# Kernel tuning notes

Hardware: AMD Instinct MI355X
Metric: run time of the kernel (lower is better)

Reference implementation:

```python
import jax, jax.numpy as jnp
import numpy as np

EPS = 1e-6  # torch.nn.CosineSimilarity eps


def _emb_sum(table, ids):
    # ids: (N, L) int -> (N, D): gather rows then sum over tokens (EmbeddingBag-sum)
    return table[ids].sum(axis=1)


def _cos_rows(q, M):
    # cosine similarity of vector q (D,) against each row of M (N, D), torch eps semantics:
    # dot / max(||a||*||b||, eps)
    num = M @ q
    den = jnp.maximum(jnp.linalg.norm(M, axis=1) * jnp.linalg.norm(q), EPS)
    return num / den


def setup_inputs() -> dict:
    key = jax.random.key(0)
    ks = jax.random.split(key, 10)
    V, D = 50000, 128
    N_MEM, N_CAND, N_PERS, L, LQ = 65536, 10000, 20, 20, 32
    return {
        "xs": jax.random.randint(ks[0], (1, LQ), 0, V, dtype=jnp.int32),
        "candidates": jax.random.randint(ks[1], (N_CAND, L), 0, V, dtype=jnp.int32),
        "persona": jax.random.randint(ks[2], (N_PERS, L), 0, V, dtype=jnp.int32),
        "keys": jax.random.randint(ks[3], (N_MEM, L), 0, V, dtype=jnp.int32),
        "values": jax.random.randint(ks[4], (N_MEM, L), 0, V, dtype=jnp.int32),
        "label": jax.random.randint(ks[5], (1, LQ), 0, V, dtype=jnp.int32),
        "shared_emb": jax.random.normal(ks[6], (V, D), dtype=jnp.float32),
        "cand_emb": jax.random.normal(ks[7], (V, D), dtype=jnp.float32),
        "R_W": jax.random.normal(ks[8], (D, D), dtype=jnp.float32) * (1.0 / np.sqrt(D)),
        "R2_W": jax.random.normal(ks[9], (D, D), dtype=jnp.float32) * (1.0 / np.sqrt(D)),
    }


def reference(xs, candidates, persona, keys, values, label, shared_emb, cand_emb, R_W, R2_W):
    enc_keys = _emb_sum(shared_emb, keys)        # (N_mem, D)
    enc_values = _emb_sum(shared_emb, values)    # (N_mem, D)
    enc_cands = _emb_sum(cand_emb, candidates)   # (N_cand, D)
    enc_pers = _emb_sum(shared_emb, persona)     # (N_pers, D)

    q = shared_emb[xs].sum(axis=1).reshape(-1)   # (D,)

    for W in (R_W, R2_W):  # loop is hardcoded to 2 hops in the source
        att = jax.nn.softmax(_cos_rows(q, enc_pers))          # (N_pers,)
        hop = (att[:, None] * enc_pers).sum(axis=0)           # (D,)
        q_plus = (q + hop) @ W.T                               # Linear no bias
        att = jax.nn.softmax(_cos_rows(q_plus, enc_keys))     # (N_mem,)
        hop = (att[:, None] * enc_values).sum(axis=0)         # (D,)
        q = (q_plus + hop) @ W.T

    preds = _cos_rows(q, enc_cands)  # (N_cand,)
    return preds
```

## Files before the change

kernel.cpp:

```cpp
#include <hip/hip_runtime.h>
#include <math.h>
#include <stdint.h>

#define D 128
#define EPS 1e-6f
typedef unsigned short u16;

#define NBK 16
#define BSTR 132
#define H1OFF 512
#define H2OFF (512 + NBK * BSTR)


__device__ __forceinline__ float wave_sum(float v) {
#pragma unroll
    for (int off = 32; off > 0; off >>= 1) v += __shfl_xor(v, off, 64);
    return v;
}
__device__ __forceinline__ float halfwave_sum(float v) {
#pragma unroll
    for (int off = 16; off > 0; off >>= 1) v += __shfl_xor(v, off, 32);
    return v;
}

__device__ __forceinline__ float bf2f(u16 h) {
    union { unsigned u; float f; } x;
    x.u = ((unsigned)h) << 16;
    return x.f;
}
__device__ __forceinline__ float bflo(unsigned u) { return bf2f((u16)(u & 0xffff)); }
__device__ __forceinline__ float bfhi(unsigned u) { return bf2f((u16)(u >> 16)); }
__device__ __forceinline__ u16 f2bf(float f) {
    union { float f; unsigned u; } x;
    x.f = f;
    unsigned u = x.u;
    return (u16)((u + 0x7fff + ((u >> 16) & 1)) >> 16);
}
__device__ __forceinline__ unsigned pack2(float a, float b) {
    return (unsigned)f2bf(a) | ((unsigned)f2bf(b) << 16);
}

__global__ void prep_k(const float* __restrict__ semb, u16* __restrict__ tbl,
                       int V, const int* __restrict__ pers, int NP,
                       const int* __restrict__ xs, int LQ,
                       float* __restrict__ enc_pers, float* __restrict__ pnorms,
                       float* __restrict__ st, int nbA) {
    const int tid = threadIdx.x;
    const int bid = blockIdx.x;
    if (bid < nbA) {
        const int n = V * 64;
        const int stride = nbA * 256;
        for (int i = bid * 256 + tid; i < n; i += stride) {
            const int v = i >> 6;
            const int c2 = i & 63;
            const float2 ab = *(const float2*)(semb + (long)v * D + 2 * c2);
            *(unsigned*)(tbl + (long)v * D + 2 * c2) = pack2(ab.x, ab.y);
        }
    } else {
        const int lane = tid & 63;
        const int half = lane >> 5;
        const int hl = lane & 31;
        const int w0 = (bid - nbA) * 4 + (tid >> 6);
        const int npr = NP + 1;
        const int npairs = (npr + 1) >> 1;
        for (int w = w0; w < npairs; w += 12) {
            const int row = 2 * w + half;
            const bool valid = row < npr;
            const int rowc = valid ? row : NP;
            const bool isq = (rowc == NP);
            const int* ids = isq ? xs : (pers + (long)rowc * 20);
            const int L = isq ? LQ : 20;
            int myid = 0;
            if (hl < L) myid = ids[hl];
            float4 acc = {0.f, 0.f, 0.f, 0.f};
            for (int t = 0; t < L; ++t) {
                const int idx = __shfl(myid, (half << 5) + t, 64);
                const float4 e = *(const float4*)(semb + (long)idx * D + 4 * hl);
                acc.x += e.x; acc.y += e.y; acc.z += e.z; acc.w += e.w;
            }
            if (valid) {
                float* outp = isq ? st : (enc_pers + (long)rowc * D);
                *(float4*)(outp + 4 * hl) = acc;
                float sq = acc.x * acc.x + acc.y * acc.y + acc.z * acc.z + acc.w * acc.w;
                sq = halfwave_sum(sq);
                if (hl == 0) {
                    if (isq) st[384] = sqrtf(sq);
                    else pnorms[rowc] = sqrtf(sq);
                }
            }
        }
    }
}

__device__ void persona_dev(const float* __restrict__ pers_rows,
                            const float* __restrict__ pnorms,
                            const float* __restrict__ W, float* __restrict__ st,
                            int NP, float* smem, int tid, int zb) {
    float* qsh = smem;
    float* qh = smem + 128;
    float* att = smem + 256;
    float* red = smem + 320;
    if (tid < D) qsh[tid] = st[tid];
    __syncthreads();
    if (tid < NP) {
        float dot = 0.f;
        const float* pr = pers_rows + (long)tid * D;
        for (int d2 = 0; d2 < D; ++d2) dot += pr[d2] * qsh[d2];
        att[tid] = dot / fmaxf(pnorms[tid] * st[384], EPS);
    }
    __syncthreads();
    if (tid == 0) {
        float m = -1e30f;
        for (int p = 0; p < NP; ++p) m = fmaxf(m, att[p]);
        float s = 0.f;
        for (int p = 0; p < NP; ++p) { att[p] = __expf(att[p] - m); s += att[p]; }
        float inv = 1.f / s;
        for (int p = 0; p < NP; ++p) att[p] *= inv;
    }
    __syncthreads();
    if (tid < D) {
        float h = 0.f;
        for (int p = 0; p < NP; ++p) h += att[p] * pers_rows[(long)p * D + tid];
        qh[tid] = qsh[tid] + h;
    }
    __syncthreads();
    float qp = 0.f;
    if (tid < D) {
        for (int d2 = 0; d2 < D; ++d2) qp += W[(long)tid * D + d2] * qh[d2];
        st[128 + tid] = qp;
    }
    float sq = wave_sum(qp * qp);
    if ((tid & 63) == 0 && tid < 128) red[tid >> 6] = sq;
    __syncthreads();
    if (tid == 0) st[385] = sqrtf(red[0] + red[1]);
    if (zb) {
        for (int i = tid; i < 2 * NBK * BSTR; i += (int)blockDim.x)
            st[H1OFF + i] = 0.f;
    } else {
        if (tid < D) st[256 + tid] = 0.f;
        if (tid == 0) st[386] = 0.f;
    }
}

__device__ void mid_dev_s(const float* __restrict__ W1, const float* __restrict__ W2,
                          const float* __restrict__ pers_rows,
                          const float* __restrict__ pnorms,
                          const float* __restrict__ st,
                          float* __restrict__ qp_out, float* __restrict__ qpn_out,
                          float* smem, int tid, int NP) {
    float* qh = smem;
    float* qsh = smem + 128;
    float* att = smem + 256;
    float* red = smem + 320;
    float esum = 0.f;
#pragma unroll
    for (int b = 0; b < NBK; ++b) esum += st[H1OFF + b * BSTR + 128];
    const float inv = 1.f / esum;
    if (tid < D) {
        float a = 0.f;
#pragma unroll
        for (int b = 0; b < NBK; ++b) a += st[H1OFF + b * BSTR + tid];
        qh[tid] = st[128 + tid] + a * inv;
    }
    __syncthreads();
    float qn = 0.f;
    if (tid < D) {
        for (int d2 = 0; d2 < D; ++d2) qn += W1[(long)tid * D + d2] * qh[d2];
        qsh[tid] = qn;
    }
    float sq = wave_sum(qn * qn);
    if ((tid & 63) == 0 && tid < 128) red[tid >> 6] = sq;
    __syncthreads();
    const float qnorm = sqrtf(red[0] + red[1]);
    if (tid < NP) {
        float dot = 0.f;
        for (int d2 = 0; d2 < D; ++d2) dot += pers_rows[(long)tid * D + d2] * qsh[d2];
        att[tid] = dot / fmaxf(pnorms[tid] * qnorm, EPS);
    }
    __syncthreads();
    if (tid == 0) {
        float m = -1e30f;
        for (int p = 0; p < NP; ++p) m = fmaxf(m, att[p]);
        float s = 0.f;
        for (int p = 0; p < NP; ++p) { att[p] = __expf(att[p] - m); s += att[p]; }
        float is = 1.f / s;
        for (int p = 0; p < NP; ++p) att[p] *= is;
    }
    __syncthreads();
    if (tid < D) {
        float h = 0.f;
        for (int p = 0; p < NP; ++p) h += att[p] * pers_rows[(long)p * D + tid];
        qh[tid] = qsh[tid] + h;
    }
    __syncthreads();
    float qp = 0.f;
    if (tid < D) {
        for (int d2 = 0; d2 < D; ++d2) qp += W2[(long)tid * D + d2] * qh[d2];
        qp_out[tid] = qp;
    }
    float sq2 = wave_sum(qp * qp);
    if ((tid & 63) == 0 && tid < 128) red[tid >> 6] = sq2;
    __syncthreads();
    if (tid == 0) *qpn_out = sqrtf(red[0] + red[1]);
    __syncthreads();
}

__global__ void kv_k(const u16* __restrict__ tbl, const int* __restrict__ kids,
                     int N, float* __restrict__ kb, float* __restrict__ knorms,
                     const float* __restrict__ enc_pers,
                     const float* __restrict__ pnorms,
                     const float* __restrict__ RW, float* __restrict__ st,
                     int NP) {
    __shared__ float smem[336];
    const int tid = threadIdx.x;
    const int bid = blockIdx.x;
    if (bid == 0) {
        persona_dev(enc_pers, pnorms, RW, st, NP, smem, tid, 1);
        return;
    }
    const int lane = tid & 63;
    const int half = lane >> 5;
    const int hl = lane & 31;
    const int ghw = ((bid - 1) * 256 + tid) >> 5;
    const int nhw = ((gridDim.x - 1) * 256) >> 5;
    for (int i = ghw; i < N; i += nhw) {
        int kid = 0;
        if (hl < 20) kid = kids[(long)i * 20 + hl];
        float k0 = 0.f, k1 = 0.f, k2 = 0.f, k3 = 0.f;
#pragma unroll
        for (int t = 0; t < 20; ++t) {
            const int kj = __shfl(kid, (half << 5) + t, 64);
            const ushort4 ke = *(const ushort4*)(tbl + (long)kj * D + 4 * hl);
            k0 += bf2f(ke.x); k1 += bf2f(ke.y); k2 += bf2f(ke.z); k3 += bf2f(ke.w);
        }
        float4 kr;
        kr.x = k0; kr.y = k1; kr.z = k2; kr.w = k3;
        *(float4*)(kb + (long)i * D + 4 * hl) = kr;
        float sq = halfwave_sum(k0 * k0 + k1 * k1 + k2 * k2 + k3 * k3);
        if (hl == 0) knorms[i] = sqrtf(sq);
    }
}

__global__ void kv_v(const u16* __restrict__ tbl, const int* __restrict__ vids,
                     int N, u16* __restrict__ vb) {
    const int tid = threadIdx.x;
    const int bid = blockIdx.x;
    const int lane = tid & 63;
    const int half = lane >> 5;
    const int hl = lane & 31;
    const int ghw = (bid * 256 + tid) >> 5;
    const int nhw = (gridDim.x * 256) >> 5;
    for (int i = ghw; i < N; i += nhw) {
        int vid = 0;
        if (hl < 20) vid = vids[(long)i * 20 + hl];
        float v0 = 0.f, v1 = 0.f, v2 = 0.f, v3 = 0.f;
#pragma unroll
        for (int t = 0; t < 20; ++t) {
            const int vj = __shfl(vid, (half << 5) + t, 64);
            const ushort4 ve = *(const ushort4*)(tbl + (long)vj * D + 4 * hl);
            v0 += bf2f(ve.x); v1 += bf2f(ve.y); v2 += bf2f(ve.z); v3 += bf2f(ve.w);
        }
        uint2 pv;
        pv.x = pack2(v0, v1);
        pv.y = pack2(v2, v3);
        *(uint2*)(vb + (long)i * D + 4 * hl) = pv;
    }
}

__global__ void attcv2_k(const float* __restrict__ kb, const u16* __restrict__ vb,
                         const float* __restrict__ knorms,
                         const float* __restrict__ W1, const float* __restrict__ W2,
                         const float* __restrict__ enc_pers,
                         const float* __restrict__ pnorms,
                         float* __restrict__ st, int N, int NP, int hop) {
    __shared__ float msm[324];
    __shared__ float qp_s[128];
    __shared__ float qpn_s;
    __shared__ float rsm[129];
    const int tid = threadIdx.x;
    if (hop == 0) {
        if (tid < 128) qp_s[tid] = st[128 + tid];
        if (tid == 0) qpn_s = st[385];
    } else {
        mid_dev_s(W1, W2, enc_pers, pnorms, st, qp_s, &qpn_s, msm, tid, NP);
    }
    __syncthreads();
    const int lane = tid & 63;
    const int half = lane >> 5;
    const int hl = lane & 31;
    const float4 qp4 = *(const float4*)(qp_s + 4 * hl);
    const float qpn = qpn_s;
    const int aoff = (hop ? H2OFF : H1OFF) + (int)(blockIdx.x & (NBK - 1)) * BSTR;
    const int ghw = (int)((blockIdx.x * blockDim.x + tid) >> 5);
    const int nhw = (int)((gridDim.x * blockDim.x) >> 5);
    float a0 = 0.f, a1 = 0.f, a2 = 0.f, a3 = 0.f;
    float esum = 0.f;
    for (int i = ghw; i < N; i += nhw) {
        const float4 kr = *(const float4*)(kb + (long)i * D + 4 * hl);
        const float part = kr.x * qp4.x + kr.y * qp4.y + kr.z * qp4.z + kr.w * qp4.w;
        const float dot = halfwave_sum(part);
        const float c = dot / fmaxf(knorms[i] * qpn, EPS);
        const float e = __expf(c);
        const uint2 vh = *(const uint2*)(vb + (long)i * D + 4 * hl);
        a0 += e * bflo(vh.x);
        a1 += e * bfhi(vh.x);
        a2 += e * bflo(vh.y);
        a3 += e * bfhi(vh.y);
        if (hl == 0) esum += e;
    }
    a0 += __shfl_xor(a0, 32, 64);
    a1 += __shfl_xor(a1, 32, 64);
    a2 += __shfl_xor(a2, 32, 64);
    a3 += __shfl_xor(a3, 32, 64);
    esum += __shfl_xor(esum, 32, 64);
    if (tid < 129) rsm[tid] = 0.f;
    __syncthreads();
    if (half == 0) {
        atomicAdd(&rsm[4 * hl + 0], a0);
        atomicAdd(&rsm[4 * hl + 1], a1);
        atomicAdd(&rsm[4 * hl + 2], a2);
        atomicAdd(&rsm[4 * hl + 3], a3);
        if (hl == 0) atomicAdd(&rsm[128], esum);
    }
    __syncthreads();
    if (tid < 128) atomicAdd(&st[aoff + tid], rsm[tid]);
    if (tid == 128) atomicAdd(&st[aoff + 128], rsm[128]);
}

__global__ void k5f(const float* __restrict__ W1, const float* __restrict__ W2,
                    const float* __restrict__ enc_pers,
                    const float* __restrict__ pnorms,
                    const float* __restrict__ cemb,
                    const int* __restrict__ cands, int NC, int NP,
                    const float* __restrict__ st, float* __restrict__ out) {
    __shared__ float msm[324];
    __shared__ float qp2_s[128];
    __shared__ float qpn2_s;
    __shared__ float qhf[128];
    __shared__ float qv[D];
    __shared__ float red2[2];
    __shared__ float qns;
    const int tid = threadIdx.x;
    mid_dev_s(W1, W2, enc_pers, pnorms, st, qp2_s, &qpn2_s, msm, tid, NP);
    float esum2 = 0.f;
#pragma unroll
    for (int b = 0; b < NBK; ++b) esum2 += st[H2OFF + b * BSTR + 128];
    const float inv2 = 1.f / esum2;
    if (tid < D) {
        float a = 0.f;
#pragma unroll
        for (int b = 0; b < NBK; ++b) a += st[H2OFF + b * BSTR + tid];
        qhf[tid] = qp2_s[tid] + a * inv2;
    }
    __syncthreads();
    float qn = 0.f;
    if (tid < D) {
        for (int d2 = 0; d2 < D; ++d2) qn += W2[(long)tid * D + d2] * qhf[d2];
        qv[tid] = qn;
    }
    float sq = wave_sum(qn * qn);
    if ((tid & 63) == 0 && tid < 128) red2[tid >> 6] = sq;
    __syncthreads();
    if (tid == 0) qns = sqrtf(red2[0] + red2[1]);
    __syncthreads();
    const int lane = tid & 63;
    const int half = lane >> 5;
    const int hl = lane & 31;
    const int gw = (int)((blockIdx.x * blockDim.x + tid) >> 6);
    const int nw = (int)((gridDim.x * blockDim.x) >> 6);
    const float4 q4 = *(const float4*)(qv + 4 * hl);
    const float qnf = qns;
    const int npair = (NC + 1) >> 1;
    for (int p = gw; p < npair; p += nw) {
        const int row = 2 * p + half;
        const bool valid = row < NC;
        const int rowc = valid ? row : (NC - 1);
        int myid = 0;
        if (hl < 20) myid = cands[(long)rowc * 20 + hl];
        float4 acc = {0.f, 0.f, 0.f, 0.f};
#pragma unroll
        for (int t = 0; t < 20; ++t) {
            const int idx = __shfl(myid, (half << 5) + t, 64);
            const float4 e = *(const float4*)(cemb + (long)idx * D + 4 * hl);
            acc.x += e.x; acc.y += e.y; acc.z += e.z; acc.w += e.w;
        }
        float dot = halfwave_sum(acc.x * q4.x + acc.y * q4.y +
                                 acc.z * q4.z + acc.w * q4.w);
        float nsq = halfwave_sum(acc.x * acc.x + acc.y * acc.y +
                                 acc.z * acc.z + acc.w * acc.w);
        if (valid && hl == 0) out[row] = dot / fmaxf(sqrtf(nsq) * qnf, EPS);
    }
}

__global__ void encode_small_p(const float* __restrict__ emb,
                               const int* __restrict__ pers, int NP, int LP,
                               const int* __restrict__ xs, int LQ,
                               float* __restrict__ pers_rows,
                               float* __restrict__ pnorms,
                               float* __restrict__ st) {
    const int lane = threadIdx.x & 63;
    const int half = lane >> 5;
    const int hl = lane & 31;
    int gw = (int)((blockIdx.x * blockDim.x + threadIdx.x) >> 6);
    int nw = (int)((gridDim.x * blockDim.x) >> 6);
    const int npr = NP + 1;
    const int npairs = (npr + 1) >> 1;
    for (int p = gw; p < npairs; p += nw) {
        const int row = 2 * p + half;
        const bool valid = row < npr;
        const int rowc = valid ? row : NP;
        const bool isq = (rowc == NP);
        const int* ids = isq ? xs : (pers + (long)rowc * LP);
        const int L = isq ? LQ : LP;
        int myid = 0;
        if (hl < L) myid = ids[hl];
        float4 acc = {0.f, 0.f, 0.f, 0.f};
        for (int t = 0; t < L; ++t) {
            const int idx = __shfl(myid, (half << 5) + t, 64);
            const float4 e = *(const float4*)(emb + (long)idx * D + 4 * hl);
            acc.x += e.x; acc.y += e.y; acc.z += e.z; acc.w += e.w;
        }
        if (valid) {
            float* outp = isq ? st : (pers_rows + (long)rowc * D);
            *(float4*)(outp + 4 * hl) = acc;
            float sq = acc.x * acc.x + acc.y * acc.y + acc.z * acc.z + acc.w * acc.w;
            sq = halfwave_sum(sq);
            if (hl == 0) {
                if (isq) st[384] = sqrtf(sq);
                else pnorms[rowc] = sqrtf(sq);
            }
        }
    }
}

__global__ void persona_hop(const float* __restrict__ pers_rows,
                            const float* __restrict__ pnorms,
                            const float* __restrict__ W,
                            float* __restrict__ st, int NP) {
    __shared__ float smem[336];
    persona_dev(pers_rows, pnorms, W, st, NP, smem, (int)threadIdx.x, 0);
}

__global__ void mid_hop(const float* __restrict__ W1, const float* __restrict__ W2,
                        const float* __restrict__ pers_rows,
                        const float* __restrict__ pnorms,
                        float* __restrict__ st, int NP) {
    __shared__ float qh[D];
    __shared__ float qsh[D];
    __shared__ float att[64];
    __shared__ float red[2];
    int tid = threadIdx.x;
    float inv = 1.f / st[386];
    qh[tid] = st[128 + tid] + st[256 + tid] * inv;
    __syncthreads();
    float qn = 0.f;
    for (int d2 = 0; d2 < D; ++d2) qn += W1[tid * D + d2] * qh[d2];
    qsh[tid] = qn;
    st[tid] = qn;
    float sq = wave_sum(qn * qn);
    if ((tid & 63) == 0) red[tid >> 6] = sq;
    __syncthreads();
    float qnorm = sqrtf(red[0] + red[1]);
    if (tid == 0) st[384] = qnorm;
    if (tid < NP) {
        float dot = 0.f;
        for (int d2 = 0; d2 < D; ++d2) dot += pers_rows[tid * D + d2] * qsh[d2];
        att[tid] = dot / fmaxf(pnorms[tid] * qnorm, EPS);
    }
    __syncthreads();
    if (tid == 0) {
        float m = -1e30f;
        for (int p = 0; p < NP; ++p) m = fmaxf(m, att[p]);
        float s = 0.f;
        for (int p = 0; p < NP; ++p) { att[p] = __expf(att[p] - m); s += att[p]; }
        float is = 1.f / s;
        for (int p = 0; p < NP; ++p) att[p] *= is;
    }
    __syncthreads();
    float h = 0.f;
    for (int p = 0; p < NP; ++p) h += att[p] * pers_rows[p * D + tid];
    qh[tid] = qsh[tid] + h;
    __syncthreads();
    float qp = 0.f;
    for (int d2 = 0; d2 < D; ++d2) qp += W2[tid * D + d2] * qh[d2];
    st[128 + tid] = qp;
    float sq2 = wave_sum(qp * qp);
    if ((tid & 63) == 0) red[tid >> 6] = sq2;
    __syncthreads();
    if (tid == 0) st[385] = sqrtf(red[0] + red[1]);
    st[256 + tid] = 0.f;
    if (tid == 0) st[386] = 0.f;
}

__global__ void finish_hop(const float* __restrict__ W, float* __restrict__ st) {
    __shared__ float qh[D];
    __shared__ float red[2];
    int tid = threadIdx.x;
    float inv = 1.f / st[386];
    qh[tid] = st[128 + tid] + st[256 + tid] * inv;
    __syncthreads();
    float qn = 0.f;
    for (int d2 = 0; d2 < D; ++d2) qn += W[tid * D + d2] * qh[d2];
    st[tid] = qn;
    float sq = wave_sum(qn * qn);
    if ((tid & 63) == 0) red[tid >> 6] = sq;
    __syncthreads();
    if (tid == 0) st[384] = sqrtf(red[0] + red[1]);
}

__global__ void k5_final(const float* __restrict__ cemb,
                         const int* __restrict__ cands, int NC,
                         const float* __restrict__ st, float* __restrict__ out) {
    const int lane = threadIdx.x & 63;
    const int half = lane >> 5;
    const int hl = lane & 31;
    const int gw = (int)((blockIdx.x * blockDim.x + threadIdx.x) >> 6);
    const int nw = (int)((gridDim.x * blockDim.x) >> 6);
    const float4 q4 = *(const float4*)(st + 4 * hl);
    const float qn = st[384];
    const int npair = (NC + 1) >> 1;
    for (int p = gw; p < npair; p += nw) {
        const int row = 2 * p + half;
        const bool valid = row < NC;
        const int rowc = valid ? row : (NC - 1);
        int myid = 0;
        if (hl < 20) myid = cands[(long)rowc * 20 + hl];
        float4 acc = {0.f, 0.f, 0.f, 0.f};
#pragma unroll
        for (int t = 0; t < 20; ++t) {
            const int idx = __shfl(myid, (half << 5) + t, 64);
            const float4 e = *(const float4*)(cemb + (long)idx * D + 4 * hl);
            acc.x += e.x; acc.y += e.y; acc.z += e.z; acc.w += e.w;
        }
        float dot = halfwave_sum(acc.x * q4.x + acc.y * q4.y +
                                 acc.z * q4.z + acc.w * q4.w);
        float nsq = halfwave_sum(acc.x * acc.x + acc.y * acc.y +
                                 acc.z * acc.z + acc.w * acc.w);
        if (valid && hl == 0) out[row] = dot / fmaxf(sqrtf(nsq) * qn, EPS);
    }
}

__global__ void big_att_rc(const float* __restrict__ emb,
                           const int* __restrict__ kids,
                           const int* __restrict__ vids,
                           float* __restrict__ st, int N) {
    __shared__ float s[129];
    const int tid = threadIdx.x;
    const int lane = tid & 63;
    const int half = lane >> 5;
    const int hl = lane & 31;
    const int gw = (int)((blockIdx.x * blockDim.x + tid) >> 6);
    const int nw = (int)((gridDim.x * blockDim.x) >> 6);
    const float4 qp = *(const float4*)(st + 128 + 4 * hl);
    const float qpn = st[385];
    float4 hacc = {0.f, 0.f, 0.f, 0.f};
    float esum = 0.f;
    const int npair = (N + 1) >> 1;
    for (int p = gw; p < npair; p += nw) {
        const int row = 2 * p + half;
        const bool valid = row < N;
        const int rowc = valid ? row : (N - 1);
        int kid = 0, vid = 0;
        if (hl < 20) {
            kid = kids[(long)rowc * 20 + hl];
            vid = vids[(long)rowc * 20 + hl];
        }
        float4 ka = {0.f, 0.f, 0.f, 0.f}, va = {0.f, 0.f, 0.f, 0.f};
#pragma unroll
        for (int t = 0; t < 20; ++t) {
            const int ki = __shfl(kid, (half << 5) + t, 64);
            const int vi = __shfl(vid, (half << 5) + t, 64);
            const float4 ke = *(const float4*)(emb + (long)ki * D + 4 * hl);
            const float4 ve = *(const float4*)(emb + (long)vi * D + 4 * hl);
            ka.x += ke.x; ka.y += ke.y; ka.z += ke.z; ka.w += ke.w;
            va.x += ve.x; va.y += ve.y; va.z += ve.z; va.w += ve.w;
        }
        float nsq = halfwave_sum(ka.x * ka.x + ka.y * ka.y + ka.z * ka.z + ka.w * ka.w);
        float dot = halfwave_sum(ka.x * qp.x + ka.y * qp.y + ka.z * qp.z + ka.w * qp.w);
        const float c = dot / fmaxf(sqrtf(nsq) * qpn, EPS);
        float e = __expf(c);
        if (!valid) e = 0.f;
        hacc.x += e * va.x; hacc.y += e * va.y;
        hacc.z += e * va.z; hacc.w += e * va.w;
        if (hl == 0) esum += e;
    }
    hacc.x += __shfl_xor(hacc.x, 32, 64);
    hacc.y += __shfl_xor(hacc.y, 32, 64);
    hacc.z += __shfl_xor(hacc.z, 32, 64);
    hacc.w += __shfl_xor(hacc.w, 32, 64);
    esum += __shfl_xor(esum, 32, 64);
    if (tid < 129) s[tid] = 0.f;
    __syncthreads();
    if (half == 0) {
        atomicAdd(&s[4 * hl + 0], hacc.x);
        atomicAdd(&s[4 * hl + 1], hacc.y);
        atomicAdd(&s[4 * hl + 2], hacc.z);
        atomicAdd(&s[4 * hl + 3], hacc.w);
        if (hl == 0) atomicAdd(&s[128], esum);
    }
    __syncthreads();
    if (tid < 128) atomicAdd(&st[256 + tid], s[tid]);
    if (tid == 128) atomicAdd(&st[386], s[128]);
}

static inline size_t align16(size_t b) { return (b + 15) & ~(size_t)15; }

extern "C" void kernel_launch(void* const* d_in, const int* in_sizes, int n_in,
                              void* d_out, int out_size, void* d_ws, size_t ws_size,
                              hipStream_t stream) {
    const int* xs = (const int*)d_in[0];
    const int* cands = (const int*)d_in[1];
    const int* pers = (const int*)d_in[2];
    const int* keys = (const int*)d_in[3];
    const int* values = (const int*)d_in[4];
    const float* semb = (const float*)d_in[6];
    const float* cemb = (const float*)d_in[7];
    const float* RW = (const float*)d_in[8];
    const float* R2W = (const float*)d_in[9];
    float* out = (float*)d_out;

    const int L = 20;
    const int LQ = in_sizes[0];
    const int VD = in_sizes[6];
    const int V = VD / D;
    const int NMEM = in_sizes[3] / L;
    const int NCAND = in_sizes[1] / L;
    const int NPERS = in_sizes[2] / L;

    size_t need = align16((size_t)VD * 2) + align16((size_t)NMEM * D * 2) +
                  align16((size_t)NMEM * D * 4) + align16((size_t)NMEM * 4) +
                  align16((size_t)NPERS * D * 4) + align16((size_t)NPERS * 4) +
                  8192 * 4;
    bool stored = (d_ws != nullptr) && (ws_size >= need) && (NMEM % 4 == 0) &&
                  (NMEM <= 65536) && ((VD & 3) == 0) && (LQ <= 32) &&
                  (NPERS <= 64);

    const int THR = 256;
    char* base = (char*)d_ws;
    u16 *tbl16 = nullptr, *vb = nullptr;
    float *kb = nullptr, *knorms = nullptr;
    if (stored) {
        tbl16 = (u16*)base;  base += align16((size_t)VD * 2);
        vb = (u16*)base;     base += align16((size_t)NMEM * D * 2);
        kb = (float*)base;   base += align16((size_t)NMEM * D * 4);
        knorms = (float*)base; base += align16((size_t)NMEM * 4);
    }
    float* enc_pers = (float*)base; base += align16((size_t)NPERS * D * 4);
    float* pnorms = (float*)base;   base += align16((size_t)NPERS * 4);
    float* st = (float*)base;

    if (stored) {
        const int nbA = 2048;
        prep_k<<<nbA + 3, THR, 0, stream>>>(semb, tbl16, V, pers, NPERS, xs, LQ,
                                            enc_pers, pnorms, st, nbA);
        kv_k<<<2049, THR, 0, stream>>>(tbl16, keys, NMEM, kb, knorms,
                                       enc_pers, pnorms, RW, st, NPERS);
        kv_v<<<2048, THR, 0, stream>>>(tbl16, values, NMEM, vb);
        attcv2_k<<<1024, THR, 0, stream>>>(kb, vb, knorms, RW, R2W, enc_pers,
                                           pnorms, st, NMEM, NPERS, 0);
        attcv2_k<<<1024, THR, 0, stream>>>(kb, vb, knorms, RW, R2W, enc_pers,
                                           pnorms, st, NMEM, NPERS, 1);
        k5f<<<640, THR, 0, stream>>>(RW, R2W, enc_pers, pnorms, cemb, cands,
                                     NCAND, NPERS, st, out);
        (void)n_in; (void)out_size;
        return;
    }

    {
        int npairs = (NPERS + 2) / 2;
        int blocks = (npairs + 3) / 4;
        encode_small_p<<<blocks, THR, 0, stream>>>(semb, pers, NPERS, L, xs,
                                                   LQ, enc_pers, pnorms, st);
    }
    persona_hop<<<1, 128, 0, stream>>>(enc_pers, pnorms, RW, st, NPERS);
    big_att_rc<<<1024, THR, 0, stream>>>(semb, keys, values, st, NMEM);
    mid_hop<<<1, 128, 0, stream>>>(RW, R2W, enc_pers, pnorms, st, NPERS);
    big_att_rc<<<1024, THR, 0, stream>>>(semb, keys, values, st, NMEM);
    finish_hop<<<1, 128, 0, stream>>>(R2W, st);
    int nblk5 = (((NCAND + 1) / 2) + 3) / 4;
    k5_final<<<nblk5, THR, 0, stream>>>(cemb, cands, NCAND, st, out);

    (void)n_in; (void)out_size;
}
```

Before: 269.1 us.

## Fuse key/value encoding with first-hop memory attention into one kernel

The separate key-encode and value-encode kernels and the first-hop attention pass are merged into one kernel. It gathers both key and value rows, computes the key norm and cosine score, and accumulates the exp-weighted values directly from registers, while still writing kb/vb/knorms for the second hop. This removes a full re-read of the encoded key and value buffers plus one launch. The price is a new one-block persona-hop kernel that must run before it, since the query is now needed up front. The partial-sum bucket count is doubled to spread the global atomics, and the workspace reservation is enlarged to match.

```diff
diff --git a/kernel.cpp b/kernel.cpp
--- a/kernel.cpp
+++ b/kernel.cpp
@@ -6,7 +6,7 @@
 #define EPS 1e-6f
 typedef unsigned short u16;
 
-#define NBK 16
+#define NBK 32
 #define BSTR 132
 #define H1OFF 512
 #define H2OFF (512 + NBK * BSTR)
@@ -142,6 +142,14 @@
     }
 }
 
+__global__ void persona_hop_s(const float* __restrict__ pers_rows,
+                              const float* __restrict__ pnorms,
+                              const float* __restrict__ W,
+                              float* __restrict__ st, int NP) {
+    __shared__ float smem[336];
+    persona_dev(pers_rows, pnorms, W, st, NP, smem, (int)threadIdx.x, 1);
+}
+
 __device__ void mid_dev_s(const float* __restrict__ W1, const float* __restrict__ W2,
                           const float* __restrict__ pers_rows,
                           const float* __restrict__ pnorms,
@@ -205,66 +213,78 @@
     __syncthreads();
 }
 
-__global__ void kv_k(const u16* __restrict__ tbl, const int* __restrict__ kids,
-                     int N, float* __restrict__ kb, float* __restrict__ knorms,
-                     const float* __restrict__ enc_pers,
-                     const float* __restrict__ pnorms,
-                     const float* __restrict__ RW, float* __restrict__ st,
-                     int NP) {
-    __shared__ float smem[336];
+__global__ void kvh1_k(const u16* __restrict__ tbl, const int* __restrict__ kids,
+                       const int* __restrict__ vids, int N,
+                       float* __restrict__ kb, u16* __restrict__ vb,
+                       float* __restrict__ knorms, float* __restrict__ st) {
+    __shared__ float qp_s[128];
+    __shared__ float qpn_s;
+    __shared__ float rsm[129];
     const int tid = threadIdx.x;
-    const int bid = blockIdx.x;
-    if (bid == 0) {
-        persona_dev(enc_pers, pnorms, RW, st, NP, smem, tid, 1);
-        return;
-    }
+    if (tid < 128) qp_s[tid] = st[128 + tid];
+    if (tid == 128) qpn_s = st[385];
+    __syncthreads();
     const int lane = tid & 63;
     const int half = lane >> 5;
     const int hl = lane & 31;
-    const int ghw = ((bid - 1) * 256 + tid) >> 5;
-    const int nhw = ((gridDim.x - 1) * 256) >> 5;
+    const float4 qp4 = *(const float4*)(qp_s + 4 * hl);
+    const float qpn = qpn_s;
+    const int ghw = (int)((blockIdx.x * blockDim.x + tid) >> 5);
+    const int nhw = (int)((gridDim.x * blockDim.x) >> 5);
+    float a0 = 0.f, a1 = 0.f, a2 = 0.f, a3 = 0.f;
+    float esum = 0.f;
     for (int i = ghw; i < N; i += nhw) {
-        int kid = 0;
-        if (hl < 20) kid = kids[(long)i * 20 + hl];
+        int kid = 0, vid = 0;
+        if (hl < 20) {
+            kid = kids[(long)i * 20 + hl];
+            vid = vids[(long)i * 20 + hl];
+        }
         float k0 = 0.f, k1 = 0.f, k2 = 0.f, k3 = 0.f;
+        float v0 = 0.f, v1 = 0.f, v2 = 0.f, v3 = 0.f;
 #pragma unroll
         for (int t = 0; t < 20; ++t) {
             const int kj = __shfl(kid, (half << 5) + t, 64);
+            const int vj = __shfl(vid, (half << 5) + t, 64);
             const ushort4 ke = *(const ushort4*)(tbl + (long)kj * D + 4 * hl);
+            const ushort4 ve = *(const ushort4*)(tbl + (long)vj * D + 4 * hl);
             k0 += bf2f(ke.x); k1 += bf2f(ke.y); k2 += bf2f(ke.z); k3 += bf2f(ke.w);
+            v0 += bf2f(ve.x); v1 += bf2f(ve.y); v2 += bf2f(ve.z); v3 += bf2f(ve.w);
         }
         float4 kr;
         kr.x = k0; kr.y = k1; kr.z = k2; kr.w = k3;
         *(float4*)(kb + (long)i * D + 4 * hl) = kr;
-        float sq = halfwave_sum(k0 * k0 + k1 * k1 + k2 * k2 + k3 * k3);
-        if (hl == 0) knorms[i] = sqrtf(sq);
-    }
-}
-
-__global__ void kv_v(const u16* __restrict__ tbl, const int* __restrict__ vids,
-                     int N, u16* __restrict__ vb) {
-    const int tid = threadIdx.x;
-    const int bid = blockIdx.x;
-    const int lane = tid & 63;
-    const int half = lane >> 5;
-    const int hl = lane & 31;
-    const int ghw = (bid * 256 + tid) >> 5;
-    const int nhw = (gridDim.x * 256) >> 5;
-    for (int i = ghw; i < N; i += nhw) {
-        int vid = 0;
-        if (hl < 20) vid = vids[(long)i * 20 + hl];
-        float v0 = 0.f, v1 = 0.f, v2 = 0.f, v3 = 0.f;
-#pragma unroll
-        for (int t = 0; t < 20; ++t) {
-            const int vj = __shfl(vid, (half << 5) + t, 64);
-            const ushort4 ve = *(const ushort4*)(tbl + (long)vj * D + 4 * hl);
-            v0 += bf2f(ve.x); v1 += bf2f(ve.y); v2 += bf2f(ve.z); v3 += bf2f(ve.w);
-        }
         uint2 pv;
         pv.x = pack2(v0, v1);
         pv.y = pack2(v2, v3);
         *(uint2*)(vb + (long)i * D + 4 * hl) = pv;
-    }
+        const float nsq = halfwave_sum(k0 * k0 + k1 * k1 + k2 * k2 + k3 * k3);
+        const float knorm = sqrtf(nsq);
+        if (hl == 0) knorms[i] = knorm;
+        const float part = k0 * qp4.x + k1 * qp4.y + k2 * qp4.z + k3 * qp4.w;
+        const float dot = halfwave_sum(part);
+        const float c = dot / fmaxf(knorm * qpn, EPS);
+        const float e = __expf(c);
+        a0 += e * v0; a1 += e * v1; a2 += e * v2; a3 += e * v3;
+        if (hl == 0) esum += e;
+    }
+    a0 += __shfl_xor(a0, 32, 64);
+    a1 += __shfl_xor(a1, 32, 64);
+    a2 += __shfl_xor(a2, 32, 64);
+    a3 += __shfl_xor(a3, 32, 64);
+    esum += __shfl_xor(esum, 32, 64);
+    if (tid < 129) rsm[tid] = 0.f;
+    __syncthreads();
+    if (half == 0) {
+        atomicAdd(&rsm[4 * hl + 0], a0);
+        atomicAdd(&rsm[4 * hl + 1], a1);
+        atomicAdd(&rsm[4 * hl + 2], a2);
+        atomicAdd(&rsm[4 * hl + 3], a3);
+        if (hl == 0) atomicAdd(&rsm[128], esum);
+    }
+    __syncthreads();
+    const int aoff = H1OFF + (int)(blockIdx.x & (NBK - 1)) * BSTR;
+    if (tid < 128) atomicAdd(&st[aoff + tid], rsm[tid]);
+    if (tid == 128) atomicAdd(&st[aoff + 128], rsm[128]);
 }
 
 __global__ void attcv2_k(const float* __restrict__ kb, const u16* __restrict__ vb,
@@ -272,25 +292,19 @@
                          const float* __restrict__ W1, const float* __restrict__ W2,
                          const float* __restrict__ enc_pers,
                          const float* __restrict__ pnorms,
-                         float* __restrict__ st, int N, int NP, int hop) {
+                         float* __restrict__ st, int N, int NP) {
     __shared__ float msm[324];
     __shared__ float qp_s[128];
     __shared__ float qpn_s;
     __shared__ float rsm[129];
     const int tid = threadIdx.x;
-    if (hop == 0) {
-        if (tid < 128) qp_s[tid] = st[128 + tid];
-        if (tid == 0) qpn_s = st[385];
-    } else {
-        mid_dev_s(W1, W2, enc_pers, pnorms, st, qp_s, &qpn_s, msm, tid, NP);
-    }
+    mid_dev_s(W1, W2, enc_pers, pnorms, st, qp_s, &qpn_s, msm, tid, NP);
     __syncthreads();
     const int lane = tid & 63;
     const int half = lane >> 5;
     const int hl = lane & 31;
     const float4 qp4 = *(const float4*)(qp_s + 4 * hl);
     const float qpn = qpn_s;
-    const int aoff = (hop ? H2OFF : H1OFF) + (int)(blockIdx.x & (NBK - 1)) * BSTR;
     const int ghw = (int)((blockIdx.x * blockDim.x + tid) >> 5);
     const int nhw = (int)((gridDim.x * blockDim.x) >> 5);
     float a0 = 0.f, a1 = 0.f, a2 = 0.f, a3 = 0.f;
@@ -323,6 +337,7 @@
         if (hl == 0) atomicAdd(&rsm[128], esum);
     }
     __syncthreads();
+    const int aoff = H2OFF + (int)(blockIdx.x & (NBK - 1)) * BSTR;
     if (tid < 128) atomicAdd(&st[aoff + tid], rsm[tid]);
     if (tid == 128) atomicAdd(&st[aoff + 128], rsm[128]);
 }
@@ -630,7 +645,7 @@
     size_t need = align16((size_t)VD * 2) + align16((size_t)NMEM * D * 2) +
                   align16((size_t)NMEM * D * 4) + align16((size_t)NMEM * 4) +
                   align16((size_t)NPERS * D * 4) + align16((size_t)NPERS * 4) +
-                  8192 * 4;
+                  16384 * 4;
     bool stored = (d_ws != nullptr) && (ws_size >= need) && (NMEM % 4 == 0) &&
                   (NMEM <= 65536) && ((VD & 3) == 0) && (LQ <= 32) &&
                   (NPERS <= 64);
@@ -653,13 +668,11 @@
         const int nbA = 2048;
         prep_k<<<nbA + 3, THR, 0, stream>>>(semb, tbl16, V, pers, NPERS, xs, LQ,
                                             enc_pers, pnorms, st, nbA);
-        kv_k<<<2049, THR, 0, stream>>>(tbl16, keys, NMEM, kb, knorms,
-                                       enc_pers, pnorms, RW, st, NPERS);
-        kv_v<<<2048, THR, 0, stream>>>(tbl16, values, NMEM, vb);
+        persona_hop_s<<<1, 128, 0, stream>>>(enc_pers, pnorms, RW, st, NPERS);
+        kvh1_k<<<2048, THR, 0, stream>>>(tbl16, keys, values, NMEM, kb, vb,
+                                         knorms, st);
         attcv2_k<<<1024, THR, 0, stream>>>(kb, vb, knorms, RW, R2W, enc_pers,
-                                           pnorms, st, NMEM, NPERS, 0);
-        attcv2_k<<<1024, THR, 0, stream>>>(kb, vb, knorms, RW, R2W, enc_pers,
-                                           pnorms, st, NMEM, NPERS, 1);
+                                           pnorms, st, NMEM, NPERS);
         k5f<<<640, THR, 0, stream>>>(RW, R2W, enc_pers, pnorms, cemb, cands,
                                      NCAND, NPERS, st, out);
         (void)n_in; (void)out_size;
```

Measured after the change: 262.0 us. 2.6% less time.
